# Optimization experiments

Measured on AMD Instinct MI355X. Metric: run time of the kernel, lower is better.

Reference implementation:

```python
import jax, jax.numpy as jnp
import numpy as np

B = 1024
INPUT_DIM = 768
NUM_CLASSES = 5
NUM_PRIMARY_CAPS = 32
PRIMARY_CAP_DIM = 8
ROUTING_CAP_DIM = 16
NUM_ITER = 3
PROJ_DIM = 256 * 6 * 6  # 9216
NUM_IN_CAPS = NUM_PRIMARY_CAPS * 16  # conv output is 4x4 spatial -> 512


def squash(t, axis=-1):
    sq = jnp.sum(t * t, axis=axis, keepdims=True)
    scale = sq / (1.0 + sq)
    return scale * t / jnp.sqrt(sq + 1e-8)


def setup_inputs() -> dict:
    key = jax.random.key(0)
    k = jax.random.split(key, 6)
    x = jax.random.normal(k[0], (B, INPUT_DIM), dtype=jnp.float32)
    W1 = jax.random.normal(k[1], (INPUT_DIM, PROJ_DIM), dtype=jnp.float32) * 0.02
    b1 = jnp.zeros((PROJ_DIM,), dtype=jnp.float32)
    convW = jax.random.normal(k[2], (NUM_PRIMARY_CAPS * PRIMARY_CAP_DIM, 256, 3, 3), dtype=jnp.float32) * 0.02  # OIHW
    convB = jnp.zeros((NUM_PRIMARY_CAPS * PRIMARY_CAP_DIM,), dtype=jnp.float32)
    # matches torch.randn init in RoutingCapsules: [num_in, num_out, out_dim, in_dim]
    Wr = jax.random.normal(k[3], (NUM_IN_CAPS, NUM_CLASSES, ROUTING_CAP_DIM, PRIMARY_CAP_DIM), dtype=jnp.float32)
    return {"x": x, "W1": W1, "b1": b1, "convW": convW, "convB": convB, "Wr": Wr}


def reference(x, W1, b1, convW, convB, Wr):
    # feature projection (dropout is identity in eval)
    h = jax.nn.relu(x @ W1 + b1)
    h = h.reshape(-1, 256, 6, 6)
    # primary capsules conv: k=3, s=1, pad=0 -> [B, 256, 4, 4]
    out = jax.lax.conv_general_dilated(h, convW, window_strides=(1, 1), padding='VALID',
                                       dimension_numbers=('NCHW', 'OIHW', 'NCHW'))
    out = out + convB[None, :, None, None]
    bsz = out.shape[0]
    out = out.reshape(bsz, NUM_PRIMARY_CAPS, PRIMARY_CAP_DIM, -1)      # [B,32,8,16]
    out = jnp.transpose(out, (0, 1, 3, 2)).reshape(bsz, -1, PRIMARY_CAP_DIM)  # [B,512,8]
    u = squash(out, axis=-1)
    # prediction vectors u_hat: [B, in_caps, out_caps, out_dim]
    u_hat = jnp.einsum('nodi,bni->bnod', Wr, u)
    # dynamic routing
    b_logits = jnp.zeros((bsz, NUM_IN_CAPS, NUM_CLASSES, 1), dtype=u_hat.dtype)
    v = None
    for it in range(NUM_ITER):
        c = jax.nn.softmax(b_logits, axis=2)
        s = jnp.sum(c * u_hat, axis=1)  # [B, out_caps, out_dim]
        v = squash(s, axis=-1)
        if it < NUM_ITER - 1:
            agreement = jnp.sum(u_hat * v[:, None], axis=-1, keepdims=True)
            b_logits = b_logits + agreement
    class_probs = jnp.sqrt(jnp.sum(v * v, axis=-1))
    return (class_probs, v)
```

## Files before the change

### kernel.cpp

```cpp
#include <hip/hip_runtime.h>
#include <hip/hip_fp16.h>

#define BSZ   1024
#define INDIM 768
#define PROJ  9216
#define NCAP  512
#define NCLS  5
#define K2    2304
#define NQ    16

typedef __bf16    bf16x8 __attribute__((ext_vector_type(8)));
typedef _Float16  f16x8  __attribute__((ext_vector_type(8)));
typedef float     f32x4  __attribute__((ext_vector_type(4)));
typedef _Float16  h2     __attribute__((ext_vector_type(2)));

static __device__ __forceinline__ unsigned short f2bf(float f) {
  unsigned int x = __float_as_uint(f);
  return (unsigned short)((x + 0x7fffu + ((x >> 16) & 1u)) >> 16);
}
static __device__ __forceinline__ unsigned short f2h(float f) {
  return __builtin_bit_cast(unsigned short, (_Float16)f);
}

#if defined(__has_builtin)
#if __has_builtin(__builtin_amdgcn_fdot2)
#define HAVE_FDOT2 1
#endif
#endif
static __device__ __forceinline__ float fdot2(h2 a, h2 b, float c) {
#ifdef HAVE_FDOT2
  return __builtin_amdgcn_fdot2(a, b, c, false);
#else
  return c + (float)a[0] * (float)b[0] + (float)a[1] * (float)b[1];
#endif
}
static __device__ __forceinline__ h2 u2h2(unsigned int u) {
  return __builtin_bit_cast(h2, u);
}

static __device__ __forceinline__ void gload16(const void* g, void* l) {
  auto gp = reinterpret_cast<const unsigned int __attribute__((address_space(1)))*>(
      (unsigned long long)g);
  auto lp = reinterpret_cast<unsigned int __attribute__((address_space(3)))*>(
      (unsigned long long)l);
  __builtin_amdgcn_global_load_lds(gp, lp, 16, 0, 0);
}

__global__ __launch_bounds__(256) void mfma_gemm_bk64(
    const unsigned short* __restrict__ A,
    const unsigned short* __restrict__ Bt,
    const float* __restrict__ bias,
    unsigned short* __restrict__ Cout,
    int M, int N, int K) {
  __shared__ __align__(16) unsigned short smem[32768];
  const int t    = threadIdx.x;
  const int bn   = blockIdx.x * 128;
  const int bm   = blockIdx.y * 128;
  const int lane = t & 63, wid = t >> 6;
  const int wm   = (wid >> 1) * 64;
  const int wn   = (wid & 1) * 64;
  const int l15  = lane & 15, kb = lane >> 4;

  const unsigned short* asrc[4];
  const unsigned short* bsrc[4];
#pragma unroll
  for (int cc = 0; cc < 4; ++cc) {
    const int c = t + cc * 256;
    const int row = c >> 3, seg = c & 7;
    const int sk = (seg ^ (row & 7)) << 3;
    asrc[cc] = A  + (size_t)(bm + row) * K + sk;
    bsrc[cc] = Bt + (size_t)(bn + row) * K + sk;
  }

  int aoff[4][2], boff[4][2];
#pragma unroll
  for (int i = 0; i < 4; ++i)
#pragma unroll
    for (int kk = 0; kk < 2; ++kk) {
      const int ra = wm + i * 16 + l15, sa = kk * 4 + kb;
      aoff[i][kk] = ra * 64 + ((sa ^ (ra & 7)) << 3);
      const int rb = wn + i * 16 + l15;
      boff[i][kk] = 8192 + rb * 64 + ((sa ^ (rb & 7)) << 3);
    }

  f32x4 acc[4][4];
#pragma unroll
  for (int i = 0; i < 4; ++i)
#pragma unroll
    for (int j = 0; j < 4; ++j)
#pragma unroll
      for (int q = 0; q < 4; ++q) acc[i][j][q] = 0.f;

  const int nk = K >> 6;
  auto stage = [&](int ks, int buf) {
    const int ko = ks << 6;
    unsigned short* sb = &smem[buf * 16384];
#pragma unroll
    for (int cc = 0; cc < 4; ++cc) {
      gload16(asrc[cc] + ko, sb + (t + cc * 256) * 8);
      gload16(bsrc[cc] + ko, sb + 8192 + (t + cc * 256) * 8);
    }
  };

  stage(0, 0);
  __syncthreads();

  int buf = 0;
  for (int ks = 0; ks < nk; ++ks) {
    if (ks + 1 < nk) stage(ks + 1, buf ^ 1);
    const unsigned short* base = &smem[buf * 16384];
    bf16x8 af[4][2], bfr[4][2];
#pragma unroll
    for (int i = 0; i < 4; ++i)
#pragma unroll
      for (int kk = 0; kk < 2; ++kk) {
        af[i][kk]  = *(const bf16x8*)(base + aoff[i][kk]);
        bfr[i][kk] = *(const bf16x8*)(base + boff[i][kk]);
      }
#pragma unroll
    for (int kk = 0; kk < 2; ++kk)
#pragma unroll
      for (int i = 0; i < 4; ++i)
#pragma unroll
        for (int j = 0; j < 4; ++j)
          acc[i][j] = __builtin_amdgcn_mfma_f32_16x16x32_bf16(af[i][kk], bfr[j][kk], acc[i][j], 0, 0, 0);
    __syncthreads();
    buf ^= 1;
  }

#pragma unroll
  for (int j = 0; j < 4; ++j) {
    const int col = bn + wn + j * 16 + l15;
    const float bv = bias[col];
#pragma unroll
    for (int i = 0; i < 4; ++i)
#pragma unroll
      for (int q = 0; q < 4; ++q) {
        const int row = bm + wm + i * 16 + kb * 4 + q;
        Cout[(size_t)row * N + col] = f2bf(fmaxf(acc[i][j][q] + bv, 0.f));
      }
  }
}

__global__ __launch_bounds__(256) void conv_gemm_sq(
    const unsigned short* __restrict__ ht,
    const unsigned short* __restrict__ Wt2,
    const float* __restrict__ convB,
    unsigned short* __restrict__ U) {
  __shared__ __align__(16) unsigned short smem[24576];
  const int t    = threadIdx.x;
  const int bn   = blockIdx.x * 128;
  const int bm   = blockIdx.y * 64;
  const int lane = t & 63, wid = t >> 6;
  const int l15  = lane & 15, kb = lane >> 4;

  const unsigned short* asrc[2];
#pragma unroll
  for (int cc = 0; cc < 2; ++cc) {
    const int c = t + cc * 256;
    const int row = c >> 3, seg = c & 7;
    const int gr = bm + row, b = gr >> 4, p = gr & 15;
    const int spb = (p >> 2) * 6 + (p & 3);
    asrc[cc] = ht + (size_t)b * PROJ + spb * 256 + ((seg ^ (row & 7)) << 3);
  }
  const unsigned short* bsrc[4];
#pragma unroll
  for (int cc = 0; cc < 4; ++cc) {
    const int c = t + cc * 256;
    const int row = c >> 3, seg = c & 7;
    bsrc[cc] = Wt2 + (size_t)(bn + row) * K2 + ((seg ^ (row & 7)) << 3);
  }

  int aoff[4][2], boff[2][2];
#pragma unroll
  for (int i = 0; i < 4; ++i)
#pragma unroll
    for (int kk = 0; kk < 2; ++kk) {
      const int row = i * 16 + l15, seg = kk * 4 + kb;
      aoff[i][kk] = row * 64 + ((seg ^ (row & 7)) << 3);
    }
#pragma unroll
  for (int j = 0; j < 2; ++j)
#pragma unroll
    for (int kk = 0; kk < 2; ++kk) {
      const int row = wid * 32 + j * 16 + l15, seg = kk * 4 + kb;
      boff[j][kk] = 4096 + row * 64 + ((seg ^ (row & 7)) << 3);
    }

  f32x4 acc[4][2];
#pragma unroll
  for (int i = 0; i < 4; ++i)
#pragma unroll
    for (int j = 0; j < 2; ++j)
#pragma unroll
      for (int q = 0; q < 4; ++q) acc[i][j][q] = 0.f;

  auto stage = [&](int ks, int buf) {
    const int tap  = ks >> 2;
    const int aofs = (tap + 3 * (tap / 3)) * 256 + ((ks & 3) << 6);
    const int bofs = ks << 6;
    unsigned short* sb = &smem[buf * 12288];
    gload16(asrc[0] + aofs, sb + t * 8);
    gload16(asrc[1] + aofs, sb + t * 8 + 2048);
    gload16(bsrc[0] + bofs, sb + 4096 + t * 8);
    gload16(bsrc[1] + bofs, sb + 4096 + t * 8 + 2048);
    gload16(bsrc[2] + bofs, sb + 4096 + t * 8 + 4096);
    gload16(bsrc[3] + bofs, sb + 4096 + t * 8 + 6144);
  };

  stage(0, 0);
  __syncthreads();

  int buf = 0;
  for (int ks = 0; ks < 36; ++ks) {
    if (ks + 1 < 36) stage(ks + 1, buf ^ 1);
    const unsigned short* base = &smem[buf * 12288];
    bf16x8 af[4][2], bfr[2][2];
#pragma unroll
    for (int i = 0; i < 4; ++i)
#pragma unroll
      for (int kk = 0; kk < 2; ++kk) af[i][kk] = *(const bf16x8*)(base + aoff[i][kk]);
#pragma unroll
    for (int j = 0; j < 2; ++j)
#pragma unroll
      for (int kk = 0; kk < 2; ++kk) bfr[j][kk] = *(const bf16x8*)(base + boff[j][kk]);
#pragma unroll
    for (int kk = 0; kk < 2; ++kk)
#pragma unroll
      for (int i = 0; i < 4; ++i)
#pragma unroll
        for (int j = 0; j < 2; ++j)
          acc[i][j] = __builtin_amdgcn_mfma_f32_16x16x32_bf16(af[i][kk], bfr[j][kk], acc[i][j], 0, 0, 0);
    __syncthreads();
    buf ^= 1;
  }

#pragma unroll
  for (int j = 0; j < 2; ++j) {
    const int oc  = bn + wid * 32 + j * 16 + l15;
    const int cap = oc >> 3, ii = oc & 7;
    const float bv = convB[oc];
#pragma unroll
    for (int i = 0; i < 4; ++i) {
#pragma unroll
      for (int q = 0; q < 4; ++q) {
        const int row = bm + i * 16 + kb * 4 + q;
        const int b = row >> 4, p = row & 15;
        const float val = acc[i][j][q] + bv;
        float sq = val * val;
        sq += __shfl_xor(sq, 1);
        sq += __shfl_xor(sq, 2);
        sq += __shfl_xor(sq, 4);
        const float scale = sq / (1.f + sq) / sqrtf(sq + 1e-8f);
        U[(size_t)b * 4096 + cap * 128 + p * 8 + ii] = f2h(val * scale);
      }
    }
  }
}

#define TP_BLOCKS (288 * 24)
#define NX_ITEMS (BSZ * INDIM / 4)
#define NW_ITEMS (NCAP * 640 / 4)
#define NWT_ITEMS (NCAP * 80)
#define NC_ITEMS 65536
#define NB_ITEMS PROJ
#define EW_TOTAL (NX_ITEMS + NW_ITEMS + NWT_ITEMS + NC_ITEMS + NB_ITEMS)
#define EW_BLOCKS (EW_TOTAL / 256)

__global__ __launch_bounds__(256) void prep_all(
    const float* __restrict__ W1, unsigned short* __restrict__ w1t,
    const float* __restrict__ x, unsigned short* __restrict__ xb,
    const float* __restrict__ Wr, __half2* __restrict__ wrh,
    unsigned short* __restrict__ wrh_t,
    const float* __restrict__ convW, unsigned short* __restrict__ wt2,
    const float* __restrict__ b1, float* __restrict__ pb1) {
  __shared__ float tile[32][33];
  if (blockIdx.x < TP_BLOCKS) {
    const int tb = blockIdx.x;
    const int n0 = (tb % 288) * 32, k0 = (tb / 288) * 32;
    const int r = threadIdx.x >> 3, c = (threadIdx.x & 7) * 4;
    float4 v = *(const float4*)(W1 + (size_t)(k0 + r) * PROJ + n0 + c);
    tile[r][c] = v.x; tile[r][c + 1] = v.y; tile[r][c + 2] = v.z; tile[r][c + 3] = v.w;
    __syncthreads();
    ushort4 o;
    o.x = f2bf(tile[c + 0][r]); o.y = f2bf(tile[c + 1][r]);
    o.z = f2bf(tile[c + 2][r]); o.w = f2bf(tile[c + 3][r]);
    const int nn = n0 + r;
    const int prow = (nn % 36) * 256 + nn / 36;
    *(ushort4*)(w1t + (size_t)prow * INDIM + k0 + c) = o;
    return;
  }
  const int id = (blockIdx.x - TP_BLOCKS) * 256 + threadIdx.x;
  if (id < NX_ITEMS) {
    float4 v = ((const float4*)x)[id];
    ushort4 o;
    o.x = f2bf(v.x); o.y = f2bf(v.y); o.z = f2bf(v.z); o.w = f2bf(v.w);
    ((ushort4*)xb)[id] = o;
  } else if (id < NX_ITEMS + NW_ITEMS) {
    const int i = id - NX_ITEMS;
    float4 v = ((const float4*)Wr)[i];
    wrh[i * 2]     = __floats2half2_rn(v.x, v.y);
    wrh[i * 2 + 1] = __floats2half2_rn(v.z, v.w);
  } else if (id < NX_ITEMS + NW_ITEMS + NWT_ITEMS) {
    const int i = id - NX_ITEMS - NW_ITEMS;
    const int od = i / NCAP, n = i % NCAP;
    const float4 a = *(const float4*)(Wr + (size_t)n * 640 + od * 8);
    const float4 b = *(const float4*)(Wr + (size_t)n * 640 + od * 8 + 4);
    __half2 h0 = __floats2half2_rn(a.x, a.y), h1 = __floats2half2_rn(a.z, a.w);
    __half2 h2v = __floats2half2_rn(b.x, b.y), h3 = __floats2half2_rn(b.z, b.w);
    uint4 st = make_uint4(__builtin_bit_cast(unsigned int, h0),
                          __builtin_bit_cast(unsigned int, h1),
                          __builtin_bit_cast(unsigned int, h2v),
                          __builtin_bit_cast(unsigned int, h3));
    *(uint4*)(wrh_t + (size_t)od * 4096 + n * 8) = st;
  } else if (id < NX_ITEMS + NW_ITEMS + NWT_ITEMS + NC_ITEMS) {
    const int i = id - NX_ITEMS - NW_ITEMS - NWT_ITEMS;
    const int oc = i >> 8, ic = i & 255;
    const float* s = convW + (size_t)i * 9;
#pragma unroll
    for (int tap = 0; tap < 9; ++tap)
      wt2[(size_t)oc * K2 + tap * 256 + ic] = f2bf(s[tap]);
  } else if (id < EW_TOTAL) {
    const int n = id - NX_ITEMS - NW_ITEMS - NWT_ITEMS - NC_ITEMS;
    pb1[(n % 36) * 256 + n / 36] = b1[n];
  }
}

__global__ __launch_bounds__(256) void s0v0_gemm(
    const unsigned short* __restrict__ U,
    const unsigned short* __restrict__ WrhT,
    float* __restrict__ v0) {
  __shared__ float red[4][16][16];
  __shared__ float sl[16][17];
  __shared__ float scl[16];
  const int bt = blockIdx.x, o = blockIdx.y;
  const int t = threadIdx.x, wid = t >> 6, lane = t & 63;
  const int l15 = lane & 15, kb = lane >> 4;
  const int gb = bt * 16;

  f32x4 acc;
  acc[0] = 0.f; acc[1] = 0.f; acc[2] = 0.f; acc[3] = 0.f;
  const unsigned short* abase = WrhT + (size_t)(o * 16 + l15) * 4096 + kb * 8;
  const unsigned short* bbase = U + (size_t)(gb + l15) * 4096 + kb * 8;
  const int k0b = wid * 1024;
#pragma unroll 4
  for (int k0 = k0b; k0 < k0b + 1024; k0 += 32) {
    const f16x8 av = __builtin_bit_cast(f16x8, *(const uint4*)(abase + k0));
    const f16x8 bv = __builtin_bit_cast(f16x8, *(const uint4*)(bbase + k0));
    acc = __builtin_amdgcn_mfma_f32_16x16x32_f16(av, bv, acc, 0, 0, 0);
  }
#pragma unroll
  for (int q = 0; q < 4; ++q) red[wid][kb * 4 + q][l15] = acc[q];
  __syncthreads();
  const int row = t >> 4, col = t & 15;
  const float s = 0.2f * (red[0][row][col] + red[1][row][col] +
                          red[2][row][col] + red[3][row][col]);
  sl[row][col] = s;
  __syncthreads();
  if (t < 16) {
    float sq = 0.f;
#pragma unroll
    for (int r = 0; r < 16; ++r) { const float xx = sl[r][t]; sq += xx * xx; }
    scl[t] = sq / (1.f + sq) / sqrtf(sq + 1e-8f);
  }
  __syncthreads();
  v0[(size_t)(gb + col) * 80 + o * 16 + row] = s * scl[col];
}

__global__ __launch_bounds__(512) void uhat_p1(
    const unsigned short* __restrict__ U,
    const unsigned short* __restrict__ Wrh,
    const float* __restrict__ v0,
    unsigned short* __restrict__ uhat,
    float* __restrict__ sp1,
    int b0, int CB) {
  __shared__ float sred[8][16][80];
  const int mt = blockIdx.x, q = blockIdx.y;
  const int t = threadIdx.x, wid = t >> 6, lane = t & 63;
  const int l15 = lane & 15, kb = lane >> 4;
  const int bm = mt * 16;
  const int gb = b0 + bm;

  f32x4 vreg[5];
#pragma unroll
  for (int jn = 0; jn < 5; ++jn)
    vreg[jn] = *(const f32x4*)(v0 + (size_t)(gb + l15) * 80 + jn * 16 + kb * 4);

  f32x4 sacc[5];
#pragma unroll
  for (int jn = 0; jn < 5; ++jn)
#pragma unroll
    for (int qq = 0; qq < 4; ++qq) sacc[jn][qq] = 0.f;

  const uint4 zz = make_uint4(0, 0, 0, 0);
#pragma unroll
  for (int i = 0; i < 4; ++i) {
    const int n = q * 32 + wid * 4 + i;
    uint4 av = zz;
    if (kb == 0) av = *(const uint4*)(U + (size_t)(gb + l15) * 4096 + n * 8);
    const f16x8 uf = __builtin_bit_cast(f16x8, av);
    f32x4 cfr[5];
#pragma unroll
    for (int jn = 0; jn < 5; ++jn) {
      uint4 wv = zz;
      if (kb == 0) wv = *(const uint4*)(Wrh + (size_t)n * 640 + (jn * 16 + l15) * 8);
      f32x4 z;
      z[0] = 0.f; z[1] = 0.f; z[2] = 0.f; z[3] = 0.f;
      cfr[jn] = __builtin_amdgcn_mfma_f32_16x16x32_f16(
          __builtin_bit_cast(f16x8, wv), uf, z, 0, 0, 0);
      ushort4 st;
      st.x = f2h(cfr[jn][0]); st.y = f2h(cfr[jn][1]);
      st.z = f2h(cfr[jn][2]); st.w = f2h(cfr[jn][3]);
      *(ushort4*)(uhat + ((size_t)(bm + l15) * 512 + n) * 80 + jn * 16 + kb * 4) = st;
    }
    float a[5];
#pragma unroll
    for (int jn = 0; jn < 5; ++jn) {
      float d = cfr[jn][0] * vreg[jn][0] + cfr[jn][1] * vreg[jn][1] +
                cfr[jn][2] * vreg[jn][2] + cfr[jn][3] * vreg[jn][3];
      d += __shfl_xor(d, 16);
      d += __shfl_xor(d, 32);
      a[jn] = d;
    }
    float m = fmaxf(fmaxf(fmaxf(a[0], a[1]), fmaxf(a[2], a[3])), a[4]);
    float c[5], es = 0.f;
#pragma unroll
    for (int o = 0; o < 5; ++o) { c[o] = __expf(a[o] - m); es += c[o]; }
    const float inv = 1.f / es;
#pragma unroll
    for (int jn = 0; jn < 5; ++jn) {
      const float cc = c[jn] * inv;
#pragma unroll
      for (int qq = 0; qq < 4; ++qq) sacc[jn][qq] += cc * cfr[jn][qq];
    }
  }

#pragma unroll
  for (int jn = 0; jn < 5; ++jn)
#pragma unroll
    for (int qq = 0; qq < 4; ++qq)
      sred[wid][l15][jn * 16 + kb * 4 + qq] = sacc[jn][qq];
  __syncthreads();
#pragma unroll
  for (int k = 0; k < 3; ++k) {
    const int id = t + k * 512;
    if (id < 1280) {
      const int bb = id / 80, od = id % 80;
      float val = 0.f;
#pragma unroll
      for (int w = 0; w < 8; ++w) val += sred[w][bb][od];
      sp1[((size_t)q * BSZ + gb + bb) * 80 + od] = val;
    }
  }
}

__global__ __launch_bounds__(128) void v01_k(
    const float* __restrict__ sp1, const float* __restrict__ v0,
    float* __restrict__ v01, int b0) {
  const int b = b0 + blockIdx.x, t = threadIdx.x;
  if (t < 80) {
    float s = 0.f;
#pragma unroll
    for (int g = 0; g < NQ; ++g) s += sp1[((size_t)g * BSZ + b) * 80 + t];
    float sq = s * s;
    sq += __shfl_xor(sq, 1);
    sq += __shfl_xor(sq, 2);
    sq += __shfl_xor(sq, 4);
    sq += __shfl_xor(sq, 8);
    const float scale = sq / (1.f + sq) / sqrtf(sq + 1e-8f);
    v01[(size_t)b * 80 + t] = v0[(size_t)b * 80 + t] + s * scale;
  }
}

__global__ __launch_bounds__(256) void route_pass2(
    const unsigned short* __restrict__ uhat,
    const float* __restrict__ vsum_in,
    float* __restrict__ out, int b0) {
  __shared__ unsigned int vph2[40];
  __shared__ float red[4][2][40];
  const int bl = blockIdx.x;
  const int b  = b0 + bl;
  const int t  = threadIdx.x;

  float v0r = 0.f;
  if (t < 80) {
    v0r = vsum_in[(size_t)b * 80 + t];
    const float vnext = __shfl_down(v0r, 1);
    if ((t & 1) == 0)
      vph2[t >> 1] = __builtin_bit_cast(unsigned int, __floats2half2_rn(v0r, vnext));
  }
  __syncthreads();

  const int p = t >> 1, h = t & 1;
  float acc[5][8];
#pragma unroll
  for (int o = 0; o < 5; ++o)
#pragma unroll
    for (int j = 0; j < 8; ++j) acc[o][j] = 0.f;

  const unsigned short* ub = uhat + (size_t)bl * 40960;
  for (int c4 = 0; c4 < 4; ++c4) {
    const int n = c4 * 128 + p;
    const unsigned short* row = ub + n * 80 + h * 8;
    uint4 uv[5];
#pragma unroll
    for (int o = 0; o < 5; ++o) uv[o] = *(const uint4*)(row + o * 16);
    float ap[5];
#pragma unroll
    for (int o = 0; o < 5; ++o) {
      const int vb = o * 8 + h * 4;
      float a = fdot2(u2h2(uv[o].x), u2h2(vph2[vb]), 0.f);
      a = fdot2(u2h2(uv[o].y), u2h2(vph2[vb + 1]), a);
      a = fdot2(u2h2(uv[o].z), u2h2(vph2[vb + 2]), a);
      a = fdot2(u2h2(uv[o].w), u2h2(vph2[vb + 3]), a);
      ap[o] = a + __shfl_xor(a, 1);
    }
    float m = ap[0];
#pragma unroll
    for (int o = 1; o < 5; ++o) m = fmaxf(m, ap[o]);
    float es = 0.f, e[5];
#pragma unroll
    for (int o = 0; o < 5; ++o) { e[o] = __expf(ap[o] - m); es += e[o]; }
    const float inv = 1.f / es;
#pragma unroll
    for (int o = 0; o < 5; ++o) {
      const float cc = e[o] * inv;
      h2 hx = u2h2(uv[o].x), hy = u2h2(uv[o].y), hz = u2h2(uv[o].z), hw = u2h2(uv[o].w);
      acc[o][0] += cc * (float)hx[0]; acc[o][1] += cc * (float)hx[1];
      acc[o][2] += cc * (float)hy[0]; acc[o][3] += cc * (float)hy[1];
      acc[o][4] += cc * (float)hz[0]; acc[o][5] += cc * (float)hz[1];
      acc[o][6] += cc * (float)hw[0]; acc[o][7] += cc * (float)hw[1];
    }
  }

#pragma unroll
  for (int off = 2; off <= 32; off <<= 1)
#pragma unroll
    for (int o = 0; o < 5; ++o)
#pragma unroll
      for (int j = 0; j < 8; ++j) acc[o][j] += __shfl_xor(acc[o][j], off);
  const int wid = t >> 6, lane = t & 63;
  if (lane < 2) {
#pragma unroll
    for (int o = 0; o < 5; ++o)
#pragma unroll
      for (int j = 0; j < 8; ++j) red[wid][lane][o * 8 + j] = acc[o][j];
  }
  __syncthreads();

  if (t < 80) {
    const int o = t >> 4, d = t & 15, hh = d >> 3, dl = d & 7;
    const int c = o * 8 + dl;
    float s = red[0][hh][c] + red[1][hh][c] + red[2][hh][c] + red[3][hh][c];
    float sq = s * s;
    sq += __shfl_xor(sq, 1);
    sq += __shfl_xor(sq, 2);
    sq += __shfl_xor(sq, 4);
    sq += __shfl_xor(sq, 8);
    const float scale = sq / (1.f + sq) / sqrtf(sq + 1e-8f);
    const float vn = s * scale;
    out[5 * BSZ + (size_t)b * 80 + t] = vn;
    float vv = vn * vn;
    vv += __shfl_xor(vv, 1);
    vv += __shfl_xor(vv, 2);
    vv += __shfl_xor(vv, 4);
    vv += __shfl_xor(vv, 8);
    if ((t & 15) == 0) out[(size_t)b * 5 + o] = sqrtf(vv);
  }
}

extern "C" void kernel_launch(void* const* d_in, const int* in_sizes, int n_in,
                              void* d_out, int out_size, void* d_ws, size_t ws_size,
                              hipStream_t stream) {
  const float* x     = (const float*)d_in[0];
  const float* W1    = (const float*)d_in[1];
  const float* b1    = (const float*)d_in[2];
  const float* convW = (const float*)d_in[3];
  const float* convB = (const float*)d_in[4];
  const float* Wr    = (const float*)d_in[5];
  float* out = (float*)d_out;

  char* base = (char*)d_ws;
  size_t off = 0;
  auto alloc = [&](size_t bytes) { size_t o = off; off = (off + bytes + 255) & ~(size_t)255; return o; };
  const size_t o_wrh  = alloc((size_t)NCAP * 640 * 2);
  const size_t o_wrt  = alloc((size_t)80 * 4096 * 2);
  const size_t o_u    = alloc((size_t)BSZ * 4096 * 2);
  const size_t o_sp1  = alloc((size_t)NQ * BSZ * 80 * 4);
  const size_t o_v0   = alloc((size_t)BSZ * 80 * 4);
  const size_t o_v01  = alloc((size_t)BSZ * 80 * 4);
  const size_t o_pool = off;
  size_t poff = o_pool;
  auto palloc = [&](size_t bytes) { size_t o = poff; poff = (poff + bytes + 255) & ~(size_t)255; return o; };
  const size_t o_ht  = palloc((size_t)BSZ * PROJ * 2);
  const size_t o_w1t = palloc((size_t)PROJ * INDIM * 2);
  const size_t o_xb  = palloc((size_t)BSZ * INDIM * 2);
  const size_t o_wt2 = palloc((size_t)256 * K2 * 2);
  const size_t o_pb1 = palloc((size_t)PROJ * 4);

  unsigned short* ht   = (unsigned short*)(base + o_ht);
  unsigned short* w1t  = (unsigned short*)(base + o_w1t);
  unsigned short* xb   = (unsigned short*)(base + o_xb);
  unsigned short* wt2  = (unsigned short*)(base + o_wt2);
  float*          pb1  = (float*)(base + o_pb1);
  unsigned short* wrh  = (unsigned short*)(base + o_wrh);
  unsigned short* wrt  = (unsigned short*)(base + o_wrt);
  unsigned short* u    = (unsigned short*)(base + o_u);
  float*          sp1  = (float*)(base + o_sp1);
  float*          v0   = (float*)(base + o_v0);
  float*          v01  = (float*)(base + o_v01);
  unsigned short* uhat = (unsigned short*)(base + o_pool);

  prep_all<<<TP_BLOCKS + EW_BLOCKS, 256, 0, stream>>>(
      W1, w1t, x, xb, Wr, (__half2*)wrh, wrt, convW, wt2, b1, pb1);

  mfma_gemm_bk64<<<dim3(PROJ / 128, BSZ / 128), 256, 0, stream>>>(
      xb, w1t, pb1, ht, BSZ, PROJ, INDIM);

  conv_gemm_sq<<<dim3(2, 256), 256, 0, stream>>>(ht, wt2, convB, u);

  s0v0_gemm<<<dim3(BSZ / 16, 5), 256, 0, stream>>>(u, wrt, v0);

  const size_t pool_sz = ws_size > o_pool ? ws_size - o_pool : 0;
  int CB = 1024;
  while (CB > 16 && (size_t)CB * 512 * 80 * 2 > pool_sz) CB >>= 1;
  for (int b0 = 0; b0 < BSZ; b0 += CB) {
    uhat_p1<<<dim3(CB / 16, NQ), 512, 0, stream>>>(u, wrh, v0, uhat, sp1, b0, CB);
    v01_k<<<CB, 128, 0, stream>>>(sp1, v0, v01, b0);
    route_pass2<<<CB, 256, 0, stream>>>(uhat, v01, out, b0);
  }
}
```

Baseline: 153.9 us.

## Store u_hat intermediate as software FP8 e4m3 and halve routing partial-sum splits

The u_hat buffer written by uhat_p1 and read by route_pass2 is now stored as software-encoded FP8 e4m3 bytes instead of fp16. This halves the bytes of the largest intermediate and relaxes the workspace chunking limit. Each uhat_p1 block now handles 8 capsules per wave instead of 4, so the grid's partial-sum dimension NQ drops from 16 to 8. The manual encode and decode adds integer ALU work, and the much coarser FP8 precision may hurt accuracy in the routing agreement and the weighted sums.

```diff
diff --git a/kernel.cpp b/kernel.cpp
--- a/kernel.cpp
+++ b/kernel.cpp
@@ -7,7 +7,7 @@
 #define NCAP  512
 #define NCLS  5
 #define K2    2304
-#define NQ    16
+#define NQ    8
 
 typedef __bf16    bf16x8 __attribute__((ext_vector_type(8)));
 typedef _Float16  f16x8  __attribute__((ext_vector_type(8)));
@@ -36,6 +36,28 @@
 }
 static __device__ __forceinline__ h2 u2h2(unsigned int u) {
   return __builtin_bit_cast(h2, u);
+}
+
+static __device__ __forceinline__ unsigned int f2e4m3(float f) {
+  const unsigned int hbits = f2h(f);
+  const unsigned int s = (hbits >> 8) & 0x80u;
+  const unsigned int mag = hbits & 0x7FFFu;
+  if (mag < 0x2400u) return s;
+  const unsigned int r = mag + 0x3Fu + ((mag >> 7) & 1u);
+  const unsigned int e = r >> 10;
+  const unsigned int m3 = (r >> 7) & 7u;
+  if (e > 23u || (e == 23u && m3 == 7u)) return s | 0x7Eu;
+  return s | ((e - 8u) << 3) | m3;
+}
+static __device__ __forceinline__ unsigned int e4m3h(unsigned int b8) {
+  const unsigned int s = (b8 & 0x80u) << 8;
+  const unsigned int em = b8 & 0x7Fu;
+  const unsigned int ex = em >> 3;
+  const unsigned int h = s | ((ex + 8u) << 10) | ((em & 7u) << 7);
+  return ex ? h : s;
+}
+static __device__ __forceinline__ h2 dec2(unsigned int lo, unsigned int hi) {
+  return u2h2(e4m3h(lo) | (e4m3h(hi) << 16));
 }
 
 static __device__ __forceinline__ void gload16(const void* g, void* l) {
@@ -371,7 +393,7 @@
     const unsigned short* __restrict__ U,
     const unsigned short* __restrict__ Wrh,
     const float* __restrict__ v0,
-    unsigned short* __restrict__ uhat,
+    unsigned char* __restrict__ uhat,
     float* __restrict__ sp1,
     int b0, int CB) {
   __shared__ float sred[8][16][80];
@@ -394,8 +416,8 @@
 
   const uint4 zz = make_uint4(0, 0, 0, 0);
 #pragma unroll
-  for (int i = 0; i < 4; ++i) {
-    const int n = q * 32 + wid * 4 + i;
+  for (int i = 0; i < 8; ++i) {
+    const int n = q * 64 + wid * 8 + i;
     uint4 av = zz;
     if (kb == 0) av = *(const uint4*)(U + (size_t)(gb + l15) * 4096 + n * 8);
     const f16x8 uf = __builtin_bit_cast(f16x8, av);
@@ -408,10 +430,11 @@
       z[0] = 0.f; z[1] = 0.f; z[2] = 0.f; z[3] = 0.f;
       cfr[jn] = __builtin_amdgcn_mfma_f32_16x16x32_f16(
           __builtin_bit_cast(f16x8, wv), uf, z, 0, 0, 0);
-      ushort4 st;
-      st.x = f2h(cfr[jn][0]); st.y = f2h(cfr[jn][1]);
-      st.z = f2h(cfr[jn][2]); st.w = f2h(cfr[jn][3]);
-      *(ushort4*)(uhat + ((size_t)(bm + l15) * 512 + n) * 80 + jn * 16 + kb * 4) = st;
+      const unsigned int pk = f2e4m3(cfr[jn][0]) |
+                              (f2e4m3(cfr[jn][1]) << 8) |
+                              (f2e4m3(cfr[jn][2]) << 16) |
+                              (f2e4m3(cfr[jn][3]) << 24);
+      *(unsigned int*)(uhat + ((size_t)(bm + l15) * 512 + n) * 80 + jn * 16 + kb * 4) = pk;
     }
     float a[5];
 #pragma unroll
@@ -473,7 +496,7 @@
 }
 
 __global__ __launch_bounds__(256) void route_pass2(
-    const unsigned short* __restrict__ uhat,
+    const unsigned char* __restrict__ uhat,
     const float* __restrict__ vsum_in,
     float* __restrict__ out, int b0) {
   __shared__ unsigned int vph2[40];
@@ -498,21 +521,27 @@
 #pragma unroll
     for (int j = 0; j < 8; ++j) acc[o][j] = 0.f;
 
-  const unsigned short* ub = uhat + (size_t)bl * 40960;
+  const unsigned char* ub = uhat + (size_t)bl * 40960;
   for (int c4 = 0; c4 < 4; ++c4) {
     const int n = c4 * 128 + p;
-    const unsigned short* row = ub + n * 80 + h * 8;
-    uint4 uv[5];
-#pragma unroll
-    for (int o = 0; o < 5; ++o) uv[o] = *(const uint4*)(row + o * 16);
+    const unsigned char* row = ub + n * 80 + h * 8;
+    h2 pv[5][4];
+#pragma unroll
+    for (int o = 0; o < 5; ++o) {
+      const uint2 q8 = *(const uint2*)(row + o * 16);
+      pv[o][0] = dec2(q8.x & 0xFFu, (q8.x >> 8) & 0xFFu);
+      pv[o][1] = dec2((q8.x >> 16) & 0xFFu, q8.x >> 24);
+      pv[o][2] = dec2(q8.y & 0xFFu, (q8.y >> 8) & 0xFFu);
+      pv[o][3] = dec2((q8.y >> 16) & 0xFFu, q8.y >> 24);
+    }
     float ap[5];
 #pragma unroll
     for (int o = 0; o < 5; ++o) {
       const int vb = o * 8 + h * 4;
-      float a = fdot2(u2h2(uv[o].x), u2h2(vph2[vb]), 0.f);
-      a = fdot2(u2h2(uv[o].y), u2h2(vph2[vb + 1]), a);
-      a = fdot2(u2h2(uv[o].z), u2h2(vph2[vb + 2]), a);
-      a = fdot2(u2h2(uv[o].w), u2h2(vph2[vb + 3]), a);
+      float a = fdot2(pv[o][0], u2h2(vph2[vb]), 0.f);
+      a = fdot2(pv[o][1], u2h2(vph2[vb + 1]), a);
+      a = fdot2(pv[o][2], u2h2(vph2[vb + 2]), a);
+      a = fdot2(pv[o][3], u2h2(vph2[vb + 3]), a);
       ap[o] = a + __shfl_xor(a, 1);
     }
     float m = ap[0];
@@ -525,11 +554,11 @@
 #pragma unroll
     for (int o = 0; o < 5; ++o) {
       const float cc = e[o] * inv;
-      h2 hx = u2h2(uv[o].x), hy = u2h2(uv[o].y), hz = u2h2(uv[o].z), hw = u2h2(uv[o].w);
-      acc[o][0] += cc * (float)hx[0]; acc[o][1] += cc * (float)hx[1];
-      acc[o][2] += cc * (float)hy[0]; acc[o][3] += cc * (float)hy[1];
-      acc[o][4] += cc * (float)hz[0]; acc[o][5] += cc * (float)hz[1];
-      acc[o][6] += cc * (float)hw[0]; acc[o][7] += cc * (float)hw[1];
+#pragma unroll
+      for (int w = 0; w < 4; ++w) {
+        acc[o][2 * w]     += cc * (float)pv[o][w][0];
+        acc[o][2 * w + 1] += cc * (float)pv[o][w][1];
+      }
     }
   }
 
@@ -609,7 +638,7 @@
   float*          sp1  = (float*)(base + o_sp1);
   float*          v0   = (float*)(base + o_v0);
   float*          v01  = (float*)(base + o_v01);
-  unsigned short* uhat = (unsigned short*)(base + o_pool);
+  unsigned char*  uhat = (unsigned char*)(base + o_pool);
 
   prep_all<<<TP_BLOCKS + EW_BLOCKS, 256, 0, stream>>>(
       W1, w1t, x, xb, Wr, (__half2*)wrh, wrt, convW, wt2, b1, pb1);
@@ -623,7 +652,7 @@
 
   const size_t pool_sz = ws_size > o_pool ? ws_size - o_pool : 0;
   int CB = 1024;
-  while (CB > 16 && (size_t)CB * 512 * 80 * 2 > pool_sz) CB >>= 1;
+  while (CB > 16 && (size_t)CB * 512 * 80 > pool_sz) CB >>= 1;
   for (int b0 = 0; b0 < BSZ; b0 += CB) {
     uhat_p1<<<dim3(CB / 16, NQ), 512, 0, stream>>>(u, wrh, v0, uhat, sp1, b0, CB);
     v01_k<<<CB, 128, 0, stream>>>(sp1, v0, v01, b0);
```

New measurement: 185.8 us. +20.7%, slower.
